# Optimization experiments

Measured on AMD Instinct MI355X. Metric: run time of the kernel, lower is better.

Reference implementation:

```python
import jax, jax.numpy as jnp
import numpy as np

N, H, M, B = 512, 64, 1024, 256
ETA = 1.0
INIT_STD = 0.01

def setup_inputs() -> dict:
    key = jax.random.key(0)
    k1, k2, k3, k4 = jax.random.split(key, 4)
    # Binary +/-1 sequences and memory (as produced upstream in the repo)
    sequences = jnp.where(jax.random.uniform(k1, (B, N)) < 0.5, -1.0, 1.0).astype(jnp.float32)
    memory = jnp.where(jax.random.uniform(k2, (M, N)) < 0.5, -1.0, 1.0).astype(jnp.float32)
    A_logits = (INIT_STD * jax.random.normal(k3, (N, H, N))).astype(jnp.float32)
    B_logits = (INIT_STD * jax.random.normal(k4, (H, N))).astype(jnp.float32)
    return {"sequences": sequences, "memory": memory, "A_logits": A_logits, "B_logits": B_logits}

def reference(sequences, memory, A_logits, B_logits):
    # Vectorized version of DAM.train_batch's loss over positions n=1..N-1.
    n_dim = sequences.shape[1]
    # Causal mask: row for position n attends to indices i < n. Rows n=1..N-1.
    ns = jnp.arange(1, n_dim)[:, None, None]            # (N-1,1,1)
    idx = jnp.arange(n_dim)[None, None, :]              # (1,1,N)
    mask = idx < ns                                      # (N-1,1,N)
    neg_inf = jnp.asarray(-jnp.inf, A_logits.dtype)
    A = jax.nn.softmax(jnp.where(mask, A_logits[1:], neg_inf), axis=-1)  # (N-1,H,N), zeros outside mask
    Bn = jax.nn.softmax(B_logits, axis=-1)               # (H,N)
    phi_mu = jnp.einsum('hn,mn->mh', Bn, memory)         # (M,H) memory keys
    hat_phi = jnp.einsum('bi,nhi->bnh', sequences, A)    # (B,N-1,H) queries for every position at once
    score = ETA * jnp.einsum('bnh,mh->bnm', hat_phi, phi_mu)  # (B,N-1,M)
    pi = jax.nn.softmax(score, axis=-1)                  # retrieval distribution over memories
    plus = (memory[:, 1:] > 0).astype(pi.dtype)          # (M,N-1): memory bit at position n is +1
    prob = jnp.einsum('bnm,mn->bn', pi, plus)            # P(next bit = +1)
    prob = jnp.clip(prob, 1e-6, 1.0 - 1e-6)
    target = (sequences[:, 1:] > 0).astype(prob.dtype)
    bce = -(target * jnp.log(prob) + (1.0 - target) * jnp.log1p(-prob))
    # mean over batch per position, summed over positions, / (N-1) == global mean
    return jnp.mean(bce)
```

## Files before the change

### kernel.cpp

```cpp
#include <hip/hip_runtime.h>
#include <stdint.h>

#define NPOS 512
#define NH   64
#define NM   1024
#define NB   256
#define NM1  511

typedef __attribute__((ext_vector_type(8)))  short bf16x8;
typedef __attribute__((ext_vector_type(16))) float f32x16;
typedef __attribute__((ext_vector_type(4)))  float f32x4;
typedef __attribute__((ext_vector_type(4)))  int   i32x4;

#if __has_builtin(__builtin_amdgcn_exp2f)
#define EXP2F(x) __builtin_amdgcn_exp2f(x)
#else
#define EXP2F(x) __expf((x) * 0.69314718055994531f)
#endif

__device__ __forceinline__ unsigned short f2bf(float x) {
    unsigned u = __float_as_uint(x);
    u = (u + 0x7FFFu + ((u >> 16) & 1u)) >> 16;
    return (unsigned short)u;
}
__device__ __forceinline__ int pack2(unsigned short a, unsigned short b) {
    return (int)a | ((int)b << 16);
}

__global__ __launch_bounds__(256, 4)
void kA_prep(const float* __restrict__ seq, const float* __restrict__ Bl,
             const float* __restrict__ mem,
             unsigned short* __restrict__ seq_bf, float* __restrict__ BnT,
             float* __restrict__ plusT, float* __restrict__ out) {
    const int bid = blockIdx.x, t = threadIdx.x;
    if (bid < 128) {
        if (bid == 0 && t == 0) out[0] = 0.f;
        int idx = (bid * 256 + t) * 4;
        f32x4 v = *(const f32x4*)(seq + idx);
        int2 o;
        o.x = pack2(f2bf(v.x), f2bf(v.y));
        o.y = pack2(f2bf(v.z), f2bf(v.w));
        *(int2*)(seq_bf + idx) = o;
    } else if (bid < 144) {
        const int h = (bid - 128) * 4 + (t >> 6), l = t & 63;
        float v[8]; float mx = -1e30f;
#pragma unroll
        for (int j = 0; j < 8; j++) { v[j] = Bl[h * NPOS + l + 64 * j]; mx = fmaxf(mx, v[j]); }
#pragma unroll
        for (int o = 32; o; o >>= 1) mx = fmaxf(mx, __shfl_xor(mx, o));
        float s = 0.f;
#pragma unroll
        for (int j = 0; j < 8; j++) { v[j] = __expf(v[j] - mx); s += v[j]; }
#pragma unroll
        for (int o = 32; o; o >>= 1) s += __shfl_xor(s, o);
        float r = 1.0f / s;
#pragma unroll
        for (int j = 0; j < 8; j++) BnT[(l + 64 * j) * NH + h] = v[j] * r;
    } else {
        __shared__ float sT[64][65];
        const int bb = bid - 144;
        const int mt = bb >> 3, nt = bb & 7;
        const int rr = t >> 2, cc = t & 3;
        const float* src = mem + (size_t)(mt * 64 + rr) * NPOS + nt * 64 + cc * 16;
#pragma unroll
        for (int j = 0; j < 4; j++) {
            f32x4 v = *(const f32x4*)(src + j * 4);
            sT[rr][cc * 16 + j * 4 + 0] = (v.x > 0.f) ? 1.f : 0.f;
            sT[rr][cc * 16 + j * 4 + 1] = (v.y > 0.f) ? 1.f : 0.f;
            sT[rr][cc * 16 + j * 4 + 2] = (v.z > 0.f) ? 1.f : 0.f;
            sT[rr][cc * 16 + j * 4 + 3] = (v.w > 0.f) ? 1.f : 0.f;
        }
        __syncthreads();
        float* dst = plusT + (size_t)(nt * 64 + rr) * NM + mt * 64 + cc * 16;
#pragma unroll
        for (int j = 0; j < 4; j++) {
            f32x4 o;
            o.x = sT[cc * 16 + j * 4 + 0][rr];
            o.y = sT[cc * 16 + j * 4 + 1][rr];
            o.z = sT[cc * 16 + j * 4 + 2][rr];
            o.w = sT[cc * 16 + j * 4 + 3][rr];
            *(f32x4*)(dst + j * 4) = o;
        }
    }
}

__global__ __launch_bounds__(256, 4)
void k1b_phimu(const float* __restrict__ BnT, const float* __restrict__ mem,
               unsigned short* __restrict__ phimu) {
    const int m0 = blockIdx.x * 2, t = threadIdx.x;
    __shared__ float mrow[2][NPOS];
    __shared__ float part[2][256];
    {
        int row = t >> 7, c = (t & 127) * 4;
        *(f32x4*)(&mrow[row][c]) = *(const f32x4*)(mem + (size_t)(m0 + row) * NPOS + c);
    }
    __syncthreads();
    const int h = t & 63, seg = t >> 6;
    float a[2] = {0.f, 0.f};
    float b2[2] = {0.f, 0.f};
    const float* bp = BnT + seg * 128 * NH + h;
#pragma unroll 8
    for (int nn = 0; nn < 128; nn += 2) {
        float x0 = bp[nn * NH], x1 = bp[(nn + 1) * NH];
#pragma unroll
        for (int row = 0; row < 2; row++) {
            a[row]  = fmaf(x0, mrow[row][seg * 128 + nn], a[row]);
            b2[row] = fmaf(x1, mrow[row][seg * 128 + nn + 1], b2[row]);
        }
    }
#pragma unroll
    for (int row = 0; row < 2; row++) part[row][t] = a[row] + b2[row];
    __syncthreads();
    if (t < 64) {
#pragma unroll
        for (int row = 0; row < 2; row++) {
            float s = (part[row][t] + part[row][t + 64]) + (part[row][t + 128] + part[row][t + 192]);
            phimu[(m0 + row) * NH + t] = f2bf(s * 1.4426950408889634f);
        }
    }
}

__global__ __launch_bounds__(256, 2)
void k23_fused(const float* __restrict__ Al, const unsigned short* __restrict__ seq_bf,
               const unsigned short* __restrict__ phimu, const float* __restrict__ plusT,
               const float* __restrict__ seq, float* __restrict__ out) {
    __shared__ __align__(16) unsigned short s_lds[256 * 72];
    __shared__ __align__(16) unsigned short e_lds[64 * 72];
    __shared__ float z_lds[64];
    __shared__ float s_plus[NM];

    const int t = threadIdx.x;
    const int n = NM1 - (int)blockIdx.x;
    const int ksteps = (n + 63) >> 6;
    const int wv = t >> 6, lane = t & 63, half = lane >> 5, r = lane & 31;

    if (t < 64) z_lds[t] = 0.f;
    *(f32x4*)(s_plus + t * 4) = *(const f32x4*)(plusT + n * NM + t * 4);

    const int eh = t >> 2, ei = (t & 3) * 16;
    const float* arow = Al + ((size_t)n * NH + eh) * NPOS + ei;
    const unsigned short* srcS = seq_bf + (size_t)t * NPOS;

    f32x16 acc00, acc01, acc10, acc11;
#pragma unroll
    for (int i = 0; i < 16; i++) { acc00[i] = 0.f; acc01[i] = 0.f; acc10[i] = 0.f; acc11[i] = 0.f; }

    f32x4 ea[4]; i32x4 sa[8];
#pragma unroll
    for (int g = 0; g < 4; g++) ea[g] = *(const f32x4*)(arow + g * 4);
#pragma unroll
    for (int c = 0; c < 8; c++) sa[c] = *(const i32x4*)(srcS + c * 8);
    __syncthreads();

    for (int kk = 0; kk < ksteps; kk++) {
        const int k0 = kk * 64;
        {
            float zp = 0.f;
            unsigned short* ep = e_lds + eh * 72 + ei;
#pragma unroll
            for (int g = 0; g < 4; g++) {
                int i0 = k0 + ei + g * 4;
                float e0 = (i0 + 0 < n) ? __expf(ea[g].x) : 0.f;
                float e1 = (i0 + 1 < n) ? __expf(ea[g].y) : 0.f;
                float e2 = (i0 + 2 < n) ? __expf(ea[g].z) : 0.f;
                float e3 = (i0 + 3 < n) ? __expf(ea[g].w) : 0.f;
                zp += (e0 + e1) + (e2 + e3);
                int2 o; o.x = pack2(f2bf(e0), f2bf(e1)); o.y = pack2(f2bf(e2), f2bf(e3));
                *(int2*)(ep + g * 4) = o;
            }
            zp += __shfl_xor(zp, 1);
            zp += __shfl_xor(zp, 2);
            if ((t & 3) == 0) z_lds[eh] += zp;
        }
        {
            unsigned short* dp = s_lds + t * 72;
#pragma unroll
            for (int c = 0; c < 8; c++) *(i32x4*)(dp + c * 8) = sa[c];
        }
        __syncthreads();
        if (kk + 1 < ksteps) {
#pragma unroll
            for (int g = 0; g < 4; g++) ea[g] = *(const f32x4*)(arow + k0 + 64 + g * 4);
#pragma unroll
            for (int c = 0; c < 8; c++) sa[c] = *(const i32x4*)(srcS + k0 + 64 + c * 8);
        }
        {
            const unsigned short* sA0 = s_lds + (wv * 64 + r) * 72;
            const unsigned short* sA1 = sA0 + 32 * 72;
            const unsigned short* sB0 = e_lds + r * 72;
            const unsigned short* sB1 = sB0 + 32 * 72;
#pragma unroll
            for (int kq = 0; kq < 4; kq++) {
                const int ko = kq * 16 + half * 8;
                bf16x8 A0 = *(const bf16x8*)(sA0 + ko);
                bf16x8 A1 = *(const bf16x8*)(sA1 + ko);
                bf16x8 B0 = *(const bf16x8*)(sB0 + ko);
                bf16x8 B1 = *(const bf16x8*)(sB1 + ko);
                acc00 = __builtin_amdgcn_mfma_f32_32x32x16_bf16(A0, B0, acc00, 0, 0, 0);
                acc01 = __builtin_amdgcn_mfma_f32_32x32x16_bf16(A0, B1, acc01, 0, 0, 0);
                acc10 = __builtin_amdgcn_mfma_f32_32x32x16_bf16(A1, B0, acc10, 0, 0, 0);
                acc11 = __builtin_amdgcn_mfma_f32_32x32x16_bf16(A1, B1, acc11, 0, 0, 0);
            }
        }
        __syncthreads();
    }
    {
        float rz0 = 1.0f / z_lds[r];
        float rz1 = 1.0f / z_lds[32 + r];
#pragma unroll
        for (int reg = 0; reg < 16; reg++) {
            int row = (reg & 3) + 8 * (reg >> 2) + 4 * half;
            s_lds[(wv * 64 + row) * 72 + r]            = f2bf(acc00[reg] * rz0);
            s_lds[(wv * 64 + row) * 72 + 32 + r]       = f2bf(acc01[reg] * rz1);
            s_lds[(wv * 64 + 32 + row) * 72 + r]       = f2bf(acc10[reg] * rz0);
            s_lds[(wv * 64 + 32 + row) * 72 + 32 + r]  = f2bf(acc11[reg] * rz1);
        }
    }
    __syncthreads();

    bf16x8 p[4];
#pragma unroll
    for (int kq = 0; kq < 4; kq++)
        p[kq] = *(const bf16x8*)(phimu + (r) * NH + kq * 16 + half * 8);
    bf16x8 q[2][4];
#pragma unroll
    for (int bs = 0; bs < 2; bs++)
#pragma unroll
        for (int kq = 0; kq < 4; kq++)
            q[bs][kq] = *(const bf16x8*)(s_lds + (wv * 64 + bs * 32 + r) * 72 + kq * 16 + half * 8);

    f32x4 den0 = {0.f,0.f,0.f,0.f}, num0 = {0.f,0.f,0.f,0.f};
    f32x4 den1 = {0.f,0.f,0.f,0.f}, num1 = {0.f,0.f,0.f,0.f};

    for (int it = 0; it < 32; ++it) {
        bf16x8 pn[4];
        if (it < 31) {
#pragma unroll
            for (int kq = 0; kq < 4; kq++)
                pn[kq] = *(const bf16x8*)(phimu + ((it + 1) * 32 + r) * NH + kq * 16 + half * 8);
        }
        f32x16 a0, a1;
#pragma unroll
        for (int i = 0; i < 16; i++) { a0[i] = 0.f; a1[i] = 0.f; }
#pragma unroll
        for (int kq = 0; kq < 4; kq++) {
            a0 = __builtin_amdgcn_mfma_f32_32x32x16_bf16(p[kq], q[0][kq], a0, 0, 0, 0);
            a1 = __builtin_amdgcn_mfma_f32_32x32x16_bf16(p[kq], q[1][kq], a1, 0, 0, 0);
        }
        const int mb = it * 32;
        f32x4 pv[4];
#pragma unroll
        for (int g = 0; g < 4; g++) pv[g] = *(const f32x4*)(s_plus + mb + 4 * half + 8 * g);
#pragma unroll
        for (int g = 0; g < 4; g++) {
            f32x4 e0, e1;
#pragma unroll
            for (int j = 0; j < 4; j++) {
                e0[j] = EXP2F(a0[4 * g + j]);
                e1[j] = EXP2F(a1[4 * g + j]);
            }
            den0 += e0; num0 += e0 * pv[g];
            den1 += e1; num1 += e1 * pv[g];
        }
        if (it < 31) {
#pragma unroll
            for (int kq = 0; kq < 4; kq++) p[kq] = pn[kq];
        }
    }
    float d0 = (den0[0] + den0[1]) + (den0[2] + den0[3]);
    float nu0 = (num0[0] + num0[1]) + (num0[2] + num0[3]);
    float d1 = (den1[0] + den1[1]) + (den1[2] + den1[3]);
    float nu1 = (num1[0] + num1[1]) + (num1[2] + num1[3]);
    d0 += __shfl_xor(d0, 32); nu0 += __shfl_xor(nu0, 32);
    d1 += __shfl_xor(d1, 32); nu1 += __shfl_xor(nu1, 32);

    float* dsum = (float*)e_lds;
    float* nsum = dsum + 256;
    if (half == 0) {
        dsum[wv * 64 + r]      = d0; nsum[wv * 64 + r]      = nu0;
        dsum[wv * 64 + 32 + r] = d1; nsum[wv * 64 + 32 + r] = nu1;
    }
    __syncthreads();
    {
        float dd = dsum[t], nn = nsum[t];
        float p2 = nn / dd;
        p2 = fminf(fmaxf(p2, 1e-6f), 1.0f - 1e-6f);
        float tg = seq[(size_t)t * NPOS + n];
        float bce = (tg > 0.f) ? -logf(p2) : -logf(1.0f - p2);
#pragma unroll
        for (int o = 32; o; o >>= 1) bce += __shfl_xor(bce, o);
        if (lane == 0) z_lds[wv] = bce;
    }
    __syncthreads();
    if (t == 0)
        atomicAdd(out, (z_lds[0] + z_lds[1] + z_lds[2] + z_lds[3]) * (1.0f / 130816.0f));
}

extern "C" void kernel_launch(void* const* d_in, const int* in_sizes, int n_in,
                              void* d_out, int out_size, void* d_ws, size_t ws_size,
                              hipStream_t stream) {
    const float* seq = (const float*)d_in[0];
    const float* mem = (const float*)d_in[1];
    const float* Al  = (const float*)d_in[2];
    const float* Bl  = (const float*)d_in[3];

    char* ws = (char*)d_ws;
    unsigned short* seq_bf = (unsigned short*)(ws + 0);
    float*          BnT    = (float*)(ws + 262144);
    unsigned short* phimu  = (unsigned short*)(ws + 393216);
    float*          plusT  = (float*)(ws + 524288);
    float*          outp   = (float*)d_out;

    kA_prep<<<272, 256, 0, stream>>>(seq, Bl, mem, seq_bf, BnT, plusT, outp);
    k1b_phimu<<<512, 256, 0, stream>>>(BnT, mem, phimu);
    k23_fused<<<511, 256, 0, stream>>>(Al, seq_bf, phimu, plusT, seq, outp);
}
```

Baseline: 145.6 us.

## Split batch across two blocks per position in fused attention-retrieval kernel

Each position is now processed by two blocks, each covering 128 batch rows, with one 32-row MFMA tile per wave instead of two. Launch bounds raise target occupancy to 4 blocks per CU and the grid doubles to 1022. The aim is better load balance of the triangular per-position workload and more latency hiding. In exchange, the softmax exponentials of A and the plus-vector loads are duplicated across the two blocks.

```diff
diff --git a/kernel.cpp b/kernel.cpp
--- a/kernel.cpp
+++ b/kernel.cpp
@@ -120,36 +120,39 @@
     }
 }
 
-__global__ __launch_bounds__(256, 2)
+__global__ __launch_bounds__(256, 4)
 void k23_fused(const float* __restrict__ Al, const unsigned short* __restrict__ seq_bf,
                const unsigned short* __restrict__ phimu, const float* __restrict__ plusT,
                const float* __restrict__ seq, float* __restrict__ out) {
-    __shared__ __align__(16) unsigned short s_lds[256 * 72];
+    __shared__ __align__(16) unsigned short s_lds[128 * 72];
     __shared__ __align__(16) unsigned short e_lds[64 * 72];
     __shared__ float z_lds[64];
     __shared__ float s_plus[NM];
 
     const int t = threadIdx.x;
-    const int n = NM1 - (int)blockIdx.x;
+    const int bid = blockIdx.x;
+    const int n = NM1 - (bid >> 1);
+    const int boff = (bid & 1) << 7;
     const int ksteps = (n + 63) >> 6;
     const int wv = t >> 6, lane = t & 63, half = lane >> 5, r = lane & 31;
 
     if (t < 64) z_lds[t] = 0.f;
-    *(f32x4*)(s_plus + t * 4) = *(const f32x4*)(plusT + n * NM + t * 4);
+    *(f32x4*)(s_plus + t * 4) = *(const f32x4*)(plusT + (size_t)n * NM + t * 4);
 
     const int eh = t >> 2, ei = (t & 3) * 16;
     const float* arow = Al + ((size_t)n * NH + eh) * NPOS + ei;
-    const unsigned short* srcS = seq_bf + (size_t)t * NPOS;
-
-    f32x16 acc00, acc01, acc10, acc11;
-#pragma unroll
-    for (int i = 0; i < 16; i++) { acc00[i] = 0.f; acc01[i] = 0.f; acc10[i] = 0.f; acc11[i] = 0.f; }
-
-    f32x4 ea[4]; i32x4 sa[8];
+    const int srow = t & 127, skh = (t >> 7) * 32;
+    const unsigned short* srcS = seq_bf + (size_t)(boff + srow) * NPOS + skh;
+
+    f32x16 acc0, acc1;
+#pragma unroll
+    for (int i = 0; i < 16; i++) { acc0[i] = 0.f; acc1[i] = 0.f; }
+
+    f32x4 ea[4]; i32x4 sa[4];
 #pragma unroll
     for (int g = 0; g < 4; g++) ea[g] = *(const f32x4*)(arow + g * 4);
 #pragma unroll
-    for (int c = 0; c < 8; c++) sa[c] = *(const i32x4*)(srcS + c * 8);
+    for (int c = 0; c < 4; c++) sa[c] = *(const i32x4*)(srcS + c * 8);
     __syncthreads();
 
     for (int kk = 0; kk < ksteps; kk++) {
@@ -173,33 +176,29 @@
             if ((t & 3) == 0) z_lds[eh] += zp;
         }
         {
-            unsigned short* dp = s_lds + t * 72;
-#pragma unroll
-            for (int c = 0; c < 8; c++) *(i32x4*)(dp + c * 8) = sa[c];
+            unsigned short* dp = s_lds + srow * 72 + skh;
+#pragma unroll
+            for (int c = 0; c < 4; c++) *(i32x4*)(dp + c * 8) = sa[c];
         }
         __syncthreads();
         if (kk + 1 < ksteps) {
 #pragma unroll
             for (int g = 0; g < 4; g++) ea[g] = *(const f32x4*)(arow + k0 + 64 + g * 4);
 #pragma unroll
-            for (int c = 0; c < 8; c++) sa[c] = *(const i32x4*)(srcS + k0 + 64 + c * 8);
+            for (int c = 0; c < 4; c++) sa[c] = *(const i32x4*)(srcS + k0 + 64 + c * 8);
         }
         {
-            const unsigned short* sA0 = s_lds + (wv * 64 + r) * 72;
-            const unsigned short* sA1 = sA0 + 32 * 72;
+            const unsigned short* sA  = s_lds + (wv * 32 + r) * 72;
             const unsigned short* sB0 = e_lds + r * 72;
             const unsigned short* sB1 = sB0 + 32 * 72;
 #pragma unroll
             for (int kq = 0; kq < 4; kq++) {
                 const int ko = kq * 16 + half * 8;
-                bf16x8 A0 = *(const bf16x8*)(sA0 + ko);
-                bf16x8 A1 = *(const bf16x8*)(sA1 + ko);
+                bf16x8 A0 = *(const bf16x8*)(sA + ko);
                 bf16x8 B0 = *(const bf16x8*)(sB0 + ko);
                 bf16x8 B1 = *(const bf16x8*)(sB1 + ko);
-                acc00 = __builtin_amdgcn_mfma_f32_32x32x16_bf16(A0, B0, acc00, 0, 0, 0);
-                acc01 = __builtin_amdgcn_mfma_f32_32x32x16_bf16(A0, B1, acc01, 0, 0, 0);
-                acc10 = __builtin_amdgcn_mfma_f32_32x32x16_bf16(A1, B0, acc10, 0, 0, 0);
-                acc11 = __builtin_amdgcn_mfma_f32_32x32x16_bf16(A1, B1, acc11, 0, 0, 0);
+                acc0 = __builtin_amdgcn_mfma_f32_32x32x16_bf16(A0, B0, acc0, 0, 0, 0);
+                acc1 = __builtin_amdgcn_mfma_f32_32x32x16_bf16(A0, B1, acc1, 0, 0, 0);
             }
         }
         __syncthreads();
@@ -210,27 +209,21 @@
 #pragma unroll
         for (int reg = 0; reg < 16; reg++) {
             int row = (reg & 3) + 8 * (reg >> 2) + 4 * half;
-            s_lds[(wv * 64 + row) * 72 + r]            = f2bf(acc00[reg] * rz0);
-            s_lds[(wv * 64 + row) * 72 + 32 + r]       = f2bf(acc01[reg] * rz1);
-            s_lds[(wv * 64 + 32 + row) * 72 + r]       = f2bf(acc10[reg] * rz0);
-            s_lds[(wv * 64 + 32 + row) * 72 + 32 + r]  = f2bf(acc11[reg] * rz1);
-        }
-    }
-    __syncthreads();
+            s_lds[(wv * 32 + row) * 72 + r]      = f2bf(acc0[reg] * rz0);
+            s_lds[(wv * 32 + row) * 72 + 32 + r] = f2bf(acc1[reg] * rz1);
+        }
+    }
 
     bf16x8 p[4];
 #pragma unroll
     for (int kq = 0; kq < 4; kq++)
-        p[kq] = *(const bf16x8*)(phimu + (r) * NH + kq * 16 + half * 8);
-    bf16x8 q[2][4];
-#pragma unroll
-    for (int bs = 0; bs < 2; bs++)
-#pragma unroll
-        for (int kq = 0; kq < 4; kq++)
-            q[bs][kq] = *(const bf16x8*)(s_lds + (wv * 64 + bs * 32 + r) * 72 + kq * 16 + half * 8);
-
-    f32x4 den0 = {0.f,0.f,0.f,0.f}, num0 = {0.f,0.f,0.f,0.f};
-    f32x4 den1 = {0.f,0.f,0.f,0.f}, num1 = {0.f,0.f,0.f,0.f};
+        p[kq] = *(const bf16x8*)(phimu + r * NH + kq * 16 + half * 8);
+    bf16x8 q[4];
+#pragma unroll
+    for (int kq = 0; kq < 4; kq++)
+        q[kq] = *(const bf16x8*)(s_lds + (wv * 32 + r) * 72 + kq * 16 + half * 8);
+
+    f32x4 den = {0.f,0.f,0.f,0.f}, num = {0.f,0.f,0.f,0.f};
 
     for (int it = 0; it < 32; ++it) {
         bf16x8 pn[4];
@@ -239,58 +232,45 @@
             for (int kq = 0; kq < 4; kq++)
                 pn[kq] = *(const bf16x8*)(phimu + ((it + 1) * 32 + r) * NH + kq * 16 + half * 8);
         }
-        f32x16 a0, a1;
-#pragma unroll
-        for (int i = 0; i < 16; i++) { a0[i] = 0.f; a1[i] = 0.f; }
-#pragma unroll
-        for (int kq = 0; kq < 4; kq++) {
-            a0 = __builtin_amdgcn_mfma_f32_32x32x16_bf16(p[kq], q[0][kq], a0, 0, 0, 0);
-            a1 = __builtin_amdgcn_mfma_f32_32x32x16_bf16(p[kq], q[1][kq], a1, 0, 0, 0);
-        }
+        f32x16 a0;
+#pragma unroll
+        for (int i = 0; i < 16; i++) a0[i] = 0.f;
+#pragma unroll
+        for (int kq = 0; kq < 4; kq++)
+            a0 = __builtin_amdgcn_mfma_f32_32x32x16_bf16(p[kq], q[kq], a0, 0, 0, 0);
         const int mb = it * 32;
-        f32x4 pv[4];
-#pragma unroll
-        for (int g = 0; g < 4; g++) pv[g] = *(const f32x4*)(s_plus + mb + 4 * half + 8 * g);
 #pragma unroll
         for (int g = 0; g < 4; g++) {
-            f32x4 e0, e1;
-#pragma unroll
-            for (int j = 0; j < 4; j++) {
-                e0[j] = EXP2F(a0[4 * g + j]);
-                e1[j] = EXP2F(a1[4 * g + j]);
-            }
-            den0 += e0; num0 += e0 * pv[g];
-            den1 += e1; num1 += e1 * pv[g];
+            f32x4 pv = *(const f32x4*)(s_plus + mb + 4 * half + 8 * g);
+            f32x4 e;
+#pragma unroll
+            for (int j = 0; j < 4; j++) e[j] = EXP2F(a0[4 * g + j]);
+            den += e; num += e * pv;
         }
         if (it < 31) {
 #pragma unroll
             for (int kq = 0; kq < 4; kq++) p[kq] = pn[kq];
         }
     }
-    float d0 = (den0[0] + den0[1]) + (den0[2] + den0[3]);
-    float nu0 = (num0[0] + num0[1]) + (num0[2] + num0[3]);
-    float d1 = (den1[0] + den1[1]) + (den1[2] + den1[3]);
-    float nu1 = (num1[0] + num1[1]) + (num1[2] + num1[3]);
-    d0 += __shfl_xor(d0, 32); nu0 += __shfl_xor(nu0, 32);
-    d1 += __shfl_xor(d1, 32); nu1 += __shfl_xor(nu1, 32);
+    float d  = (den[0] + den[1]) + (den[2] + den[3]);
+    float nu = (num[0] + num[1]) + (num[2] + num[3]);
+    d += __shfl_xor(d, 32); nu += __shfl_xor(nu, 32);
 
     float* dsum = (float*)e_lds;
-    float* nsum = dsum + 256;
-    if (half == 0) {
-        dsum[wv * 64 + r]      = d0; nsum[wv * 64 + r]      = nu0;
-        dsum[wv * 64 + 32 + r] = d1; nsum[wv * 64 + 32 + r] = nu1;
-    }
-    __syncthreads();
-    {
-        float dd = dsum[t], nn = nsum[t];
-        float p2 = nn / dd;
+    float* nsum = dsum + 128;
+    if (half == 0) { dsum[wv * 32 + r] = d; nsum[wv * 32 + r] = nu; }
+    __syncthreads();
+    float bce = 0.f;
+    if (t < 128) {
+        float dd = dsum[t], nn2 = nsum[t];
+        float p2 = nn2 / dd;
         p2 = fminf(fmaxf(p2, 1e-6f), 1.0f - 1e-6f);
-        float tg = seq[(size_t)t * NPOS + n];
-        float bce = (tg > 0.f) ? -logf(p2) : -logf(1.0f - p2);
-#pragma unroll
-        for (int o = 32; o; o >>= 1) bce += __shfl_xor(bce, o);
-        if (lane == 0) z_lds[wv] = bce;
-    }
+        float tg = seq[(size_t)(boff + t) * NPOS + n];
+        bce = (tg > 0.f) ? -logf(p2) : -logf(1.0f - p2);
+    }
+#pragma unroll
+    for (int o = 32; o; o >>= 1) bce += __shfl_xor(bce, o);
+    if (lane == 0) z_lds[wv] = bce;
     __syncthreads();
     if (t == 0)
         atomicAdd(out, (z_lds[0] + z_lds[1] + z_lds[2] + z_lds[3]) * (1.0f / 130816.0f));
@@ -313,5 +293,5 @@
 
     kA_prep<<<272, 256, 0, stream>>>(seq, Bl, mem, seq_bf, BnT, plusT, outp);
     k1b_phimu<<<512, 256, 0, stream>>>(BnT, mem, phimu);
-    k23_fused<<<511, 256, 0, stream>>>(Al, seq_bf, phimu, plusT, seq, outp);
-}
+    k23_fused<<<1022, 256, 0, stream>>>(Al, seq_bf, phimu, plusT, seq, outp);
+}
```

Result: slower. 179.5 us (+23.3%).

## Keep sequence operands in registers, double-buffer exp tiles, software-pipeline retrieval MFMAs

Applied to the files above, without the earlier changes.

Sequence tiles are now loaded from global memory straight into MFMA operand registers instead of being staged through LDS. The exponentiated A tile is double-buffered, so each k-step needs one barrier instead of two. The retrieval phase is software-pipelined so the MFMA for one phimu tile overlaps the exp/sum of the previous one. The aim is less LDS traffic and fewer barriers and stalls, at the cost of more registers. The final q writes to q_lds followed by reads from other rows have no barrier between them, since each wave reads only its own rows, which relies on the wave-local layout.

```diff
diff --git a/kernel.cpp b/kernel.cpp
--- a/kernel.cpp
+++ b/kernel.cpp
@@ -120,12 +120,45 @@
     }
 }
 
+__device__ __forceinline__ void p2_load(bf16x8 (&p)[4], const unsigned short* __restrict__ phimu,
+                                        int tile, int r, int half) {
+#pragma unroll
+    for (int kq = 0; kq < 4; kq++)
+        p[kq] = *(const bf16x8*)(phimu + (size_t)(tile * 32 + r) * NH + kq * 16 + half * 8);
+}
+__device__ __forceinline__ void p2_mfma(const bf16x8 (&p)[4], const bf16x8 (&q0)[4], const bf16x8 (&q1)[4],
+                                        f32x16& a0, f32x16& a1) {
+#pragma unroll
+    for (int i = 0; i < 16; i++) { a0[i] = 0.f; a1[i] = 0.f; }
+#pragma unroll
+    for (int kq = 0; kq < 4; kq++) {
+        a0 = __builtin_amdgcn_mfma_f32_32x32x16_bf16(p[kq], q0[kq], a0, 0, 0, 0);
+        a1 = __builtin_amdgcn_mfma_f32_32x32x16_bf16(p[kq], q1[kq], a1, 0, 0, 0);
+    }
+}
+__device__ __forceinline__ void p2_expsum(const f32x16& a0, const f32x16& a1, const float* s_plus,
+                                          int mb, int half,
+                                          f32x4& den0, f32x4& num0, f32x4& den1, f32x4& num1) {
+#pragma unroll
+    for (int g = 0; g < 4; g++) {
+        f32x4 pv = *(const f32x4*)(s_plus + mb + 4 * half + 8 * g);
+        f32x4 e0, e1;
+#pragma unroll
+        for (int j = 0; j < 4; j++) {
+            e0[j] = EXP2F(a0[4 * g + j]);
+            e1[j] = EXP2F(a1[4 * g + j]);
+        }
+        den0 += e0; num0 += e0 * pv;
+        den1 += e1; num1 += e1 * pv;
+    }
+}
+
 __global__ __launch_bounds__(256, 2)
 void k23_fused(const float* __restrict__ Al, const unsigned short* __restrict__ seq_bf,
                const unsigned short* __restrict__ phimu, const float* __restrict__ plusT,
                const float* __restrict__ seq, float* __restrict__ out) {
-    __shared__ __align__(16) unsigned short s_lds[256 * 72];
-    __shared__ __align__(16) unsigned short e_lds[64 * 72];
+    __shared__ __align__(16) unsigned short e_lds[2][64 * 72];
+    __shared__ __align__(16) unsigned short q_lds[256 * 72];
     __shared__ float z_lds[64];
     __shared__ float s_plus[NM];
 
@@ -135,28 +168,34 @@
     const int wv = t >> 6, lane = t & 63, half = lane >> 5, r = lane & 31;
 
     if (t < 64) z_lds[t] = 0.f;
-    *(f32x4*)(s_plus + t * 4) = *(const f32x4*)(plusT + n * NM + t * 4);
+    *(f32x4*)(s_plus + t * 4) = *(const f32x4*)(plusT + (size_t)n * NM + t * 4);
 
     const int eh = t >> 2, ei = (t & 3) * 16;
     const float* arow = Al + ((size_t)n * NH + eh) * NPOS + ei;
-    const unsigned short* srcS = seq_bf + (size_t)t * NPOS;
+    const unsigned short* s0 = seq_bf + (size_t)(wv * 64 + r) * NPOS;
+    const unsigned short* s1 = seq_bf + (size_t)(wv * 64 + 32 + r) * NPOS;
 
     f32x16 acc00, acc01, acc10, acc11;
 #pragma unroll
     for (int i = 0; i < 16; i++) { acc00[i] = 0.f; acc01[i] = 0.f; acc10[i] = 0.f; acc11[i] = 0.f; }
 
-    f32x4 ea[4]; i32x4 sa[8];
+    f32x4 ea[4];
+    bf16x8 sc0[4], sc1[4], sn0[4], sn1[4];
 #pragma unroll
     for (int g = 0; g < 4; g++) ea[g] = *(const f32x4*)(arow + g * 4);
 #pragma unroll
-    for (int c = 0; c < 8; c++) sa[c] = *(const i32x4*)(srcS + c * 8);
+    for (int kq = 0; kq < 4; kq++) {
+        sc0[kq] = *(const bf16x8*)(s0 + kq * 16 + half * 8);
+        sc1[kq] = *(const bf16x8*)(s1 + kq * 16 + half * 8);
+    }
     __syncthreads();
 
     for (int kk = 0; kk < ksteps; kk++) {
         const int k0 = kk * 64;
+        unsigned short* ebuf = e_lds[kk & 1];
         {
             float zp = 0.f;
-            unsigned short* ep = e_lds + eh * 72 + ei;
+            unsigned short* ep = ebuf + eh * 72 + ei;
 #pragma unroll
             for (int g = 0; g < 4; g++) {
                 int i0 = k0 + ei + g * 4;
@@ -172,37 +211,36 @@
             zp += __shfl_xor(zp, 2);
             if ((t & 3) == 0) z_lds[eh] += zp;
         }
+        if (kk + 1 < ksteps) {
+#pragma unroll
+            for (int g = 0; g < 4; g++) ea[g] = *(const f32x4*)(arow + k0 + 64 + g * 4);
+#pragma unroll
+            for (int kq = 0; kq < 4; kq++) {
+                sn0[kq] = *(const bf16x8*)(s0 + k0 + 64 + kq * 16 + half * 8);
+                sn1[kq] = *(const bf16x8*)(s1 + k0 + 64 + kq * 16 + half * 8);
+            }
+        }
+        asm volatile("s_waitcnt lgkmcnt(0)" ::: "memory");
+        __builtin_amdgcn_s_barrier();
+        asm volatile("" ::: "memory");
         {
-            unsigned short* dp = s_lds + t * 72;
-#pragma unroll
-            for (int c = 0; c < 8; c++) *(i32x4*)(dp + c * 8) = sa[c];
-        }
-        __syncthreads();
-        if (kk + 1 < ksteps) {
-#pragma unroll
-            for (int g = 0; g < 4; g++) ea[g] = *(const f32x4*)(arow + k0 + 64 + g * 4);
-#pragma unroll
-            for (int c = 0; c < 8; c++) sa[c] = *(const i32x4*)(srcS + k0 + 64 + c * 8);
-        }
-        {
-            const unsigned short* sA0 = s_lds + (wv * 64 + r) * 72;
-            const unsigned short* sA1 = sA0 + 32 * 72;
-            const unsigned short* sB0 = e_lds + r * 72;
+            const unsigned short* sB0 = ebuf + r * 72;
             const unsigned short* sB1 = sB0 + 32 * 72;
 #pragma unroll
             for (int kq = 0; kq < 4; kq++) {
                 const int ko = kq * 16 + half * 8;
-                bf16x8 A0 = *(const bf16x8*)(sA0 + ko);
-                bf16x8 A1 = *(const bf16x8*)(sA1 + ko);
                 bf16x8 B0 = *(const bf16x8*)(sB0 + ko);
                 bf16x8 B1 = *(const bf16x8*)(sB1 + ko);
-                acc00 = __builtin_amdgcn_mfma_f32_32x32x16_bf16(A0, B0, acc00, 0, 0, 0);
-                acc01 = __builtin_amdgcn_mfma_f32_32x32x16_bf16(A0, B1, acc01, 0, 0, 0);
-                acc10 = __builtin_amdgcn_mfma_f32_32x32x16_bf16(A1, B0, acc10, 0, 0, 0);
-                acc11 = __builtin_amdgcn_mfma_f32_32x32x16_bf16(A1, B1, acc11, 0, 0, 0);
+                acc00 = __builtin_amdgcn_mfma_f32_32x32x16_bf16(sc0[kq], B0, acc00, 0, 0, 0);
+                acc01 = __builtin_amdgcn_mfma_f32_32x32x16_bf16(sc0[kq], B1, acc01, 0, 0, 0);
+                acc10 = __builtin_amdgcn_mfma_f32_32x32x16_bf16(sc1[kq], B0, acc10, 0, 0, 0);
+                acc11 = __builtin_amdgcn_mfma_f32_32x32x16_bf16(sc1[kq], B1, acc11, 0, 0, 0);
             }
         }
-        __syncthreads();
+        if (kk + 1 < ksteps) {
+#pragma unroll
+            for (int kq = 0; kq < 4; kq++) { sc0[kq] = sn0[kq]; sc1[kq] = sn1[kq]; }
+        }
     }
     {
         float rz0 = 1.0f / z_lds[r];
@@ -210,63 +248,37 @@
 #pragma unroll
         for (int reg = 0; reg < 16; reg++) {
             int row = (reg & 3) + 8 * (reg >> 2) + 4 * half;
-            s_lds[(wv * 64 + row) * 72 + r]            = f2bf(acc00[reg] * rz0);
-            s_lds[(wv * 64 + row) * 72 + 32 + r]       = f2bf(acc01[reg] * rz1);
-            s_lds[(wv * 64 + 32 + row) * 72 + r]       = f2bf(acc10[reg] * rz0);
-            s_lds[(wv * 64 + 32 + row) * 72 + 32 + r]  = f2bf(acc11[reg] * rz1);
-        }
-    }
-    __syncthreads();
-
-    bf16x8 p[4];
-#pragma unroll
-    for (int kq = 0; kq < 4; kq++)
-        p[kq] = *(const bf16x8*)(phimu + (r) * NH + kq * 16 + half * 8);
-    bf16x8 q[2][4];
-#pragma unroll
-    for (int bs = 0; bs < 2; bs++)
-#pragma unroll
-        for (int kq = 0; kq < 4; kq++)
-            q[bs][kq] = *(const bf16x8*)(s_lds + (wv * 64 + bs * 32 + r) * 72 + kq * 16 + half * 8);
+            q_lds[(wv * 64 + row) * 72 + r]            = f2bf(acc00[reg] * rz0);
+            q_lds[(wv * 64 + row) * 72 + 32 + r]       = f2bf(acc01[reg] * rz1);
+            q_lds[(wv * 64 + 32 + row) * 72 + r]       = f2bf(acc10[reg] * rz0);
+            q_lds[(wv * 64 + 32 + row) * 72 + 32 + r]  = f2bf(acc11[reg] * rz1);
+        }
+    }
+
+    bf16x8 pA[4], pB[4];
+    p2_load(pA, phimu, 0, r, half);
+    p2_load(pB, phimu, 1, r, half);
+    bf16x8 q0[4], q1[4];
+#pragma unroll
+    for (int kq = 0; kq < 4; kq++) {
+        q0[kq] = *(const bf16x8*)(q_lds + (wv * 64 + r) * 72 + kq * 16 + half * 8);
+        q1[kq] = *(const bf16x8*)(q_lds + (wv * 64 + 32 + r) * 72 + kq * 16 + half * 8);
+    }
 
     f32x4 den0 = {0.f,0.f,0.f,0.f}, num0 = {0.f,0.f,0.f,0.f};
     f32x4 den1 = {0.f,0.f,0.f,0.f}, num1 = {0.f,0.f,0.f,0.f};
-
-    for (int it = 0; it < 32; ++it) {
-        bf16x8 pn[4];
-        if (it < 31) {
-#pragma unroll
-            for (int kq = 0; kq < 4; kq++)
-                pn[kq] = *(const bf16x8*)(phimu + ((it + 1) * 32 + r) * NH + kq * 16 + half * 8);
-        }
-        f32x16 a0, a1;
-#pragma unroll
-        for (int i = 0; i < 16; i++) { a0[i] = 0.f; a1[i] = 0.f; }
-#pragma unroll
-        for (int kq = 0; kq < 4; kq++) {
-            a0 = __builtin_amdgcn_mfma_f32_32x32x16_bf16(p[kq], q[0][kq], a0, 0, 0, 0);
-            a1 = __builtin_amdgcn_mfma_f32_32x32x16_bf16(p[kq], q[1][kq], a1, 0, 0, 0);
-        }
-        const int mb = it * 32;
-        f32x4 pv[4];
-#pragma unroll
-        for (int g = 0; g < 4; g++) pv[g] = *(const f32x4*)(s_plus + mb + 4 * half + 8 * g);
-#pragma unroll
-        for (int g = 0; g < 4; g++) {
-            f32x4 e0, e1;
-#pragma unroll
-            for (int j = 0; j < 4; j++) {
-                e0[j] = EXP2F(a0[4 * g + j]);
-                e1[j] = EXP2F(a1[4 * g + j]);
-            }
-            den0 += e0; num0 += e0 * pv[g];
-            den1 += e1; num1 += e1 * pv[g];
-        }
-        if (it < 31) {
-#pragma unroll
-            for (int kq = 0; kq < 4; kq++) p[kq] = pn[kq];
-        }
-    }
+    f32x16 aA0, aA1, aB0, aB1;
+
+    p2_mfma(pA, q0, q1, aA0, aA1);
+    for (int it = 0; it < 32; it += 2) {
+        if (it + 2 < 32) p2_load(pA, phimu, it + 2, r, half);
+        p2_mfma(pB, q0, q1, aB0, aB1);
+        if (it + 3 < 32) p2_load(pB, phimu, it + 3, r, half);
+        p2_expsum(aA0, aA1, s_plus, it * 32, half, den0, num0, den1, num1);
+        if (it + 2 < 32) p2_mfma(pA, q0, q1, aA0, aA1);
+        p2_expsum(aB0, aB1, s_plus, (it + 1) * 32, half, den0, num0, den1, num1);
+    }
+
     float d0 = (den0[0] + den0[1]) + (den0[2] + den0[3]);
     float nu0 = (num0[0] + num0[1]) + (num0[2] + num0[3]);
     float d1 = (den1[0] + den1[1]) + (den1[2] + den1[3]);
```

Result: no change. 148.4 us (+1.9%).

## Precompute masked exp of A_logits in prep kernel and pair blocks by workload

Applied to the files above, without the earlier changes.

Moves the masked exponentiation of A_logits into the prep kernel, writing bf16 exp values and per-head normalizers to workspace. The main kernel then streams these with register double-buffering and applies the 1/Z softmax scale after the first matmul instead of normalizing inline. Block order is interleaved so long and short causal positions alternate for load balance. The cost is an extra round trip of about 33MB of bf16 exp data through global memory. The new path only runs when the workspace is large enough.

```diff
diff --git a/kernel.cpp b/kernel.cpp
--- a/kernel.cpp
+++ b/kernel.cpp
@@ -26,6 +26,276 @@
 __device__ __forceinline__ int pack2(unsigned short a, unsigned short b) {
     return (int)a | ((int)b << 16);
 }
+
+
+__global__ __launch_bounds__(256, 4)
+void kAE_prep(const float* __restrict__ seq, const float* __restrict__ Bl,
+              const float* __restrict__ mem, const float* __restrict__ Al,
+              unsigned short* __restrict__ seq_bf, float* __restrict__ BnT,
+              float* __restrict__ plusT, unsigned short* __restrict__ Ew,
+              float* __restrict__ Zb, float* __restrict__ out) {
+    const int bid = blockIdx.x, t = threadIdx.x;
+    if (bid < 128) {
+        if (bid == 0 && t == 0) out[0] = 0.f;
+        int idx = (bid * 256 + t) * 4;
+        f32x4 v = *(const f32x4*)(seq + idx);
+        int2 o;
+        o.x = pack2(f2bf(v.x), f2bf(v.y));
+        o.y = pack2(f2bf(v.z), f2bf(v.w));
+        *(int2*)(seq_bf + idx) = o;
+    } else if (bid < 144) {
+        const int h = (bid - 128) * 4 + (t >> 6), l = t & 63;
+        float v[8]; float mx = -1e30f;
+#pragma unroll
+        for (int j = 0; j < 8; j++) { v[j] = Bl[h * NPOS + l + 64 * j]; mx = fmaxf(mx, v[j]); }
+#pragma unroll
+        for (int o = 32; o; o >>= 1) mx = fmaxf(mx, __shfl_xor(mx, o));
+        float s = 0.f;
+#pragma unroll
+        for (int j = 0; j < 8; j++) { v[j] = __expf(v[j] - mx); s += v[j]; }
+#pragma unroll
+        for (int o = 32; o; o >>= 1) s += __shfl_xor(s, o);
+        float r = 1.0f / s;
+#pragma unroll
+        for (int j = 0; j < 8; j++) BnT[(l + 64 * j) * NH + h] = v[j] * r;
+    } else if (bid < 272) {
+        __shared__ float sT[64][65];
+        const int bb = bid - 144;
+        const int mt = bb >> 3, nt = bb & 7;
+        const int rr = t >> 2, cc = t & 3;
+        const float* src = mem + (size_t)(mt * 64 + rr) * NPOS + nt * 64 + cc * 16;
+#pragma unroll
+        for (int j = 0; j < 4; j++) {
+            f32x4 v = *(const f32x4*)(src + j * 4);
+            sT[rr][cc * 16 + j * 4 + 0] = (v.x > 0.f) ? 1.f : 0.f;
+            sT[rr][cc * 16 + j * 4 + 1] = (v.y > 0.f) ? 1.f : 0.f;
+            sT[rr][cc * 16 + j * 4 + 2] = (v.z > 0.f) ? 1.f : 0.f;
+            sT[rr][cc * 16 + j * 4 + 3] = (v.w > 0.f) ? 1.f : 0.f;
+        }
+        __syncthreads();
+        float* dst = plusT + (size_t)(nt * 64 + rr) * NM + mt * 64 + cc * 16;
+#pragma unroll
+        for (int j = 0; j < 4; j++) {
+            f32x4 o;
+            o.x = sT[cc * 16 + j * 4 + 0][rr];
+            o.y = sT[cc * 16 + j * 4 + 1][rr];
+            o.z = sT[cc * 16 + j * 4 + 2][rr];
+            o.w = sT[cc * 16 + j * 4 + 3][rr];
+            *(f32x4*)(dst + j * 4) = o;
+        }
+    } else {
+        const int n = bid - 271;
+        const int h = t >> 2, j = t & 3;
+        const int lim = ((n + 63) >> 6) * 64;
+        const float* Ar = Al + ((size_t)n * NH + h) * NPOS;
+        unsigned short* Er = Ew + (size_t)(n - 1) * 32768 + h * 64;
+        float zp = 0.f;
+#pragma unroll 4
+        for (int g = 0; g < 16; g++) {
+            const int i0 = g * 32 + j * 8;
+            if (g * 32 >= lim) break;
+            f32x4 v0 = *(const f32x4*)(Ar + i0);
+            f32x4 v1 = *(const f32x4*)(Ar + i0 + 4);
+            float e0 = (i0 + 0 < n) ? __expf(v0.x) : 0.f;
+            float e1 = (i0 + 1 < n) ? __expf(v0.y) : 0.f;
+            float e2 = (i0 + 2 < n) ? __expf(v0.z) : 0.f;
+            float e3 = (i0 + 3 < n) ? __expf(v0.w) : 0.f;
+            float e4 = (i0 + 4 < n) ? __expf(v1.x) : 0.f;
+            float e5 = (i0 + 5 < n) ? __expf(v1.y) : 0.f;
+            float e6 = (i0 + 6 < n) ? __expf(v1.z) : 0.f;
+            float e7 = (i0 + 7 < n) ? __expf(v1.w) : 0.f;
+            zp += ((e0 + e1) + (e2 + e3)) + ((e4 + e5) + (e6 + e7));
+            i32x4 w;
+            w.x = pack2(f2bf(e0), f2bf(e1));
+            w.y = pack2(f2bf(e2), f2bf(e3));
+            w.z = pack2(f2bf(e4), f2bf(e5));
+            w.w = pack2(f2bf(e6), f2bf(e7));
+            *(i32x4*)(Er + (i0 >> 6) * 4096 + (i0 & 63)) = w;
+        }
+        zp += __shfl_xor(zp, 1);
+        zp += __shfl_xor(zp, 2);
+        if (j == 0) Zb[(n - 1) * 64 + h] = zp;
+    }
+}
+
+__device__ __forceinline__ void p2_load(bf16x8 (&p)[4], const unsigned short* __restrict__ phimu,
+                                        int tile, int r, int half) {
+#pragma unroll
+    for (int kq = 0; kq < 4; kq++)
+        p[kq] = *(const bf16x8*)(phimu + (size_t)(tile * 32 + r) * NH + kq * 16 + half * 8);
+}
+__device__ __forceinline__ void p2_mfma(const bf16x8 (&p)[4], const bf16x8 (&q0)[4], const bf16x8 (&q1)[4],
+                                        const f32x16& z, f32x16& a0, f32x16& a1) {
+    a0 = __builtin_amdgcn_mfma_f32_32x32x16_bf16(p[0], q0[0], z, 0, 0, 0);
+    a1 = __builtin_amdgcn_mfma_f32_32x32x16_bf16(p[0], q1[0], z, 0, 0, 0);
+#pragma unroll
+    for (int kq = 1; kq < 4; kq++) {
+        a0 = __builtin_amdgcn_mfma_f32_32x32x16_bf16(p[kq], q0[kq], a0, 0, 0, 0);
+        a1 = __builtin_amdgcn_mfma_f32_32x32x16_bf16(p[kq], q1[kq], a1, 0, 0, 0);
+    }
+}
+__device__ __forceinline__ void p2_expsum(const f32x16& a0, const f32x16& a1, const float* s_plus,
+                                          int mb, int half,
+                                          f32x4& den0, f32x4& num0, f32x4& den1, f32x4& num1) {
+#pragma unroll
+    for (int g = 0; g < 4; g++) {
+        f32x4 pv = *(const f32x4*)(s_plus + mb + 4 * half + 8 * g);
+        f32x4 e0, e1;
+#pragma unroll
+        for (int j = 0; j < 4; j++) {
+            e0[j] = EXP2F(a0[4 * g + j]);
+            e1[j] = EXP2F(a1[4 * g + j]);
+        }
+        den0 += e0; num0 += e0 * pv;
+        den1 += e1; num1 += e1 * pv;
+    }
+}
+
+__global__ __launch_bounds__(256, 2)
+void k23_fusedE(const unsigned short* __restrict__ Ew, const float* __restrict__ Zb,
+                const unsigned short* __restrict__ seq_bf,
+                const unsigned short* __restrict__ phimu, const float* __restrict__ plusT,
+                const float* __restrict__ seq, float* __restrict__ out) {
+    __shared__ __align__(16) unsigned short e_lds[2][64 * 72];
+    __shared__ __align__(16) unsigned short q_lds[256 * 72];
+    __shared__ float s_plus[NM];
+    __shared__ float w_lds[4];
+
+    const int t = threadIdx.x;
+    const int c = blockIdx.x >> 1;
+    const int n = (blockIdx.x & 1) ? (1 + c) : (NM1 - c);
+    const int ksteps = (n + 63) >> 6;
+    const int wv = t >> 6, lane = t & 63, half = lane >> 5, r = lane & 31;
+
+    *(f32x4*)(s_plus + t * 4) = *(const f32x4*)(plusT + (size_t)n * NM + t * 4);
+    const float Zr0 = Zb[(n - 1) * 64 + r];
+    const float Zr1 = Zb[(n - 1) * 64 + 32 + r];
+
+    const unsigned short* Eb = Ew + (size_t)(n - 1) * 32768;
+    const int eh = t >> 2, ec = (t & 3) * 16;
+    const unsigned short* s0 = seq_bf + (size_t)(wv * 64 + r) * NPOS;
+    const unsigned short* s1 = seq_bf + (size_t)(wv * 64 + 32 + r) * NPOS;
+
+    f32x16 acc00, acc01, acc10, acc11;
+#pragma unroll
+    for (int i = 0; i < 16; i++) { acc00[i] = 0.f; acc01[i] = 0.f; acc10[i] = 0.f; acc11[i] = 0.f; }
+
+    bf16x8 er0, er1, sc0[4], sc1[4], sn0[4], sn1[4];
+    er0 = *(const bf16x8*)(Eb + eh * 64 + ec);
+    er1 = *(const bf16x8*)(Eb + eh * 64 + ec + 8);
+#pragma unroll
+    for (int kq = 0; kq < 4; kq++) {
+        sc0[kq] = *(const bf16x8*)(s0 + kq * 16 + half * 8);
+        sc1[kq] = *(const bf16x8*)(s1 + kq * 16 + half * 8);
+    }
+
+    for (int kk = 0; kk < ksteps; kk++) {
+        {
+            unsigned short* ep = (unsigned short*)e_lds[kk & 1] + eh * 72 + ec;
+            *(bf16x8*)(ep)     = er0;
+            *(bf16x8*)(ep + 8) = er1;
+        }
+        if (kk + 1 < ksteps) {
+            const unsigned short* nb = Eb + (kk + 1) * 4096 + eh * 64 + ec;
+            er0 = *(const bf16x8*)(nb);
+            er1 = *(const bf16x8*)(nb + 8);
+            const int k0 = (kk + 1) * 64;
+#pragma unroll
+            for (int kq = 0; kq < 4; kq++) {
+                sn0[kq] = *(const bf16x8*)(s0 + k0 + kq * 16 + half * 8);
+                sn1[kq] = *(const bf16x8*)(s1 + k0 + kq * 16 + half * 8);
+            }
+        }
+        asm volatile("s_waitcnt lgkmcnt(0)" ::: "memory");
+        __builtin_amdgcn_s_barrier();
+        asm volatile("" ::: "memory");
+        {
+            const unsigned short* sB0 = (const unsigned short*)e_lds[kk & 1] + r * 72;
+            const unsigned short* sB1 = sB0 + 32 * 72;
+#pragma unroll
+            for (int kq = 0; kq < 4; kq++) {
+                const int ko = kq * 16 + half * 8;
+                bf16x8 B0 = *(const bf16x8*)(sB0 + ko);
+                bf16x8 B1 = *(const bf16x8*)(sB1 + ko);
+                acc00 = __builtin_amdgcn_mfma_f32_32x32x16_bf16(sc0[kq], B0, acc00, 0, 0, 0);
+                acc01 = __builtin_amdgcn_mfma_f32_32x32x16_bf16(sc0[kq], B1, acc01, 0, 0, 0);
+                acc10 = __builtin_amdgcn_mfma_f32_32x32x16_bf16(sc1[kq], B0, acc10, 0, 0, 0);
+                acc11 = __builtin_amdgcn_mfma_f32_32x32x16_bf16(sc1[kq], B1, acc11, 0, 0, 0);
+            }
+        }
+        if (kk + 1 < ksteps) {
+#pragma unroll
+            for (int kq = 0; kq < 4; kq++) { sc0[kq] = sn0[kq]; sc1[kq] = sn1[kq]; }
+        }
+    }
+    {
+        float rz0 = 1.0f / Zr0;
+        float rz1 = 1.0f / Zr1;
+#pragma unroll
+        for (int reg = 0; reg < 16; reg++) {
+            int row = (reg & 3) + 8 * (reg >> 2) + 4 * half;
+            q_lds[(wv * 64 + row) * 72 + r]            = f2bf(acc00[reg] * rz0);
+            q_lds[(wv * 64 + row) * 72 + 32 + r]       = f2bf(acc01[reg] * rz1);
+            q_lds[(wv * 64 + 32 + row) * 72 + r]       = f2bf(acc10[reg] * rz0);
+            q_lds[(wv * 64 + 32 + row) * 72 + 32 + r]  = f2bf(acc11[reg] * rz1);
+        }
+    }
+
+    bf16x8 p[4], pn[4];
+    p2_load(p, phimu, 0, r, half);
+    bf16x8 q0[4], q1[4];
+#pragma unroll
+    for (int kq = 0; kq < 4; kq++) {
+        q0[kq] = *(const bf16x8*)(q_lds + (wv * 64 + r) * 72 + kq * 16 + half * 8);
+        q1[kq] = *(const bf16x8*)(q_lds + (wv * 64 + 32 + r) * 72 + kq * 16 + half * 8);
+    }
+    f32x16 zacc;
+#pragma unroll
+    for (int i = 0; i < 16; i++) zacc[i] = 0.f;
+
+    f32x4 den0 = {0.f,0.f,0.f,0.f}, num0 = {0.f,0.f,0.f,0.f};
+    f32x4 den1 = {0.f,0.f,0.f,0.f}, num1 = {0.f,0.f,0.f,0.f};
+    f32x16 a0, a1;
+
+    for (int it = 0; it < 32; ++it) {
+        if (it < 31) p2_load(pn, phimu, it + 1, r, half);
+        p2_mfma(p, q0, q1, zacc, a0, a1);
+        p2_expsum(a0, a1, s_plus, it * 32, half, den0, num0, den1, num1);
+        if (it < 31) {
+#pragma unroll
+            for (int kq = 0; kq < 4; kq++) p[kq] = pn[kq];
+        }
+    }
+
+    float d0 = (den0[0] + den0[1]) + (den0[2] + den0[3]);
+    float nu0 = (num0[0] + num0[1]) + (num0[2] + num0[3]);
+    float d1 = (den1[0] + den1[1]) + (den1[2] + den1[3]);
+    float nu1 = (num1[0] + num1[1]) + (num1[2] + num1[3]);
+    d0 += __shfl_xor(d0, 32); nu0 += __shfl_xor(nu0, 32);
+    d1 += __shfl_xor(d1, 32); nu1 += __shfl_xor(nu1, 32);
+
+    float* dsum = (float*)e_lds;
+    float* nsum = dsum + 256;
+    if (half == 0) {
+        dsum[wv * 64 + r]      = d0; nsum[wv * 64 + r]      = nu0;
+        dsum[wv * 64 + 32 + r] = d1; nsum[wv * 64 + 32 + r] = nu1;
+    }
+    __syncthreads();
+    {
+        float dd = dsum[t], nn = nsum[t];
+        float p2 = nn / dd;
+        p2 = fminf(fmaxf(p2, 1e-6f), 1.0f - 1e-6f);
+        float tg = seq[(size_t)t * NPOS + n];
+        float bce = (tg > 0.f) ? -logf(p2) : -logf(1.0f - p2);
+#pragma unroll
+        for (int o = 32; o; o >>= 1) bce += __shfl_xor(bce, o);
+        if (lane == 0) w_lds[wv] = bce;
+    }
+    __syncthreads();
+    if (t == 0)
+        atomicAdd(out, (w_lds[0] + w_lds[1] + w_lds[2] + w_lds[3]) * (1.0f / 130816.0f));
+}
+
 
 __global__ __launch_bounds__(256, 4)
 void kA_prep(const float* __restrict__ seq, const float* __restrict__ Bl,
@@ -84,46 +354,10 @@
     }
 }
 
-__global__ __launch_bounds__(256, 4)
-void k1b_phimu(const float* __restrict__ BnT, const float* __restrict__ mem,
-               unsigned short* __restrict__ phimu) {
-    const int m0 = blockIdx.x * 2, t = threadIdx.x;
-    __shared__ float mrow[2][NPOS];
-    __shared__ float part[2][256];
-    {
-        int row = t >> 7, c = (t & 127) * 4;
-        *(f32x4*)(&mrow[row][c]) = *(const f32x4*)(mem + (size_t)(m0 + row) * NPOS + c);
-    }
-    __syncthreads();
-    const int h = t & 63, seg = t >> 6;
-    float a[2] = {0.f, 0.f};
-    float b2[2] = {0.f, 0.f};
-    const float* bp = BnT + seg * 128 * NH + h;
-#pragma unroll 8
-    for (int nn = 0; nn < 128; nn += 2) {
-        float x0 = bp[nn * NH], x1 = bp[(nn + 1) * NH];
-#pragma unroll
-        for (int row = 0; row < 2; row++) {
-            a[row]  = fmaf(x0, mrow[row][seg * 128 + nn], a[row]);
-            b2[row] = fmaf(x1, mrow[row][seg * 128 + nn + 1], b2[row]);
-        }
-    }
-#pragma unroll
-    for (int row = 0; row < 2; row++) part[row][t] = a[row] + b2[row];
-    __syncthreads();
-    if (t < 64) {
-#pragma unroll
-        for (int row = 0; row < 2; row++) {
-            float s = (part[row][t] + part[row][t + 64]) + (part[row][t + 128] + part[row][t + 192]);
-            phimu[(m0 + row) * NH + t] = f2bf(s * 1.4426950408889634f);
-        }
-    }
-}
-
 __global__ __launch_bounds__(256, 2)
-void k23_fused(const float* __restrict__ Al, const unsigned short* __restrict__ seq_bf,
-               const unsigned short* __restrict__ phimu, const float* __restrict__ plusT,
-               const float* __restrict__ seq, float* __restrict__ out) {
+void k23_fused0(const float* __restrict__ Al, const unsigned short* __restrict__ seq_bf,
+                const unsigned short* __restrict__ phimu, const float* __restrict__ plusT,
+                const float* __restrict__ seq, float* __restrict__ out) {
     __shared__ __align__(16) unsigned short s_lds[256 * 72];
     __shared__ __align__(16) unsigned short e_lds[64 * 72];
     __shared__ float z_lds[64];
@@ -296,6 +530,42 @@
         atomicAdd(out, (z_lds[0] + z_lds[1] + z_lds[2] + z_lds[3]) * (1.0f / 130816.0f));
 }
 
+__global__ __launch_bounds__(256, 4)
+void k1b_phimu(const float* __restrict__ BnT, const float* __restrict__ mem,
+               unsigned short* __restrict__ phimu) {
+    const int m0 = blockIdx.x * 2, t = threadIdx.x;
+    __shared__ float mrow[2][NPOS];
+    __shared__ float part[2][256];
+    {
+        int row = t >> 7, c = (t & 127) * 4;
+        *(f32x4*)(&mrow[row][c]) = *(const f32x4*)(mem + (size_t)(m0 + row) * NPOS + c);
+    }
+    __syncthreads();
+    const int h = t & 63, seg = t >> 6;
+    float a[2] = {0.f, 0.f};
+    float b2[2] = {0.f, 0.f};
+    const float* bp = BnT + seg * 128 * NH + h;
+#pragma unroll 8
+    for (int nn = 0; nn < 128; nn += 2) {
+        float x0 = bp[nn * NH], x1 = bp[(nn + 1) * NH];
+#pragma unroll
+        for (int row = 0; row < 2; row++) {
+            a[row]  = fmaf(x0, mrow[row][seg * 128 + nn], a[row]);
+            b2[row] = fmaf(x1, mrow[row][seg * 128 + nn + 1], b2[row]);
+        }
+    }
+#pragma unroll
+    for (int row = 0; row < 2; row++) part[row][t] = a[row] + b2[row];
+    __syncthreads();
+    if (t < 64) {
+#pragma unroll
+        for (int row = 0; row < 2; row++) {
+            float s = (part[row][t] + part[row][t + 64]) + (part[row][t + 128] + part[row][t + 192]);
+            phimu[(m0 + row) * NH + t] = f2bf(s * 1.4426950408889634f);
+        }
+    }
+}
+
 extern "C" void kernel_launch(void* const* d_in, const int* in_sizes, int n_in,
                               void* d_out, int out_size, void* d_ws, size_t ws_size,
                               hipStream_t stream) {
@@ -309,9 +579,19 @@
     float*          BnT    = (float*)(ws + 262144);
     unsigned short* phimu  = (unsigned short*)(ws + 393216);
     float*          plusT  = (float*)(ws + 524288);
+    float*          Zb     = (float*)(ws + 2621440);
+    unsigned short* Ew     = (unsigned short*)(ws + 2752512);
     float*          outp   = (float*)d_out;
 
-    kA_prep<<<272, 256, 0, stream>>>(seq, Bl, mem, seq_bf, BnT, plusT, outp);
-    k1b_phimu<<<512, 256, 0, stream>>>(BnT, mem, phimu);
-    k23_fused<<<511, 256, 0, stream>>>(Al, seq_bf, phimu, plusT, seq, outp);
-}
+    const size_t WS_NEEDED_E = 2752512 + (size_t)NM1 * 32768 * sizeof(unsigned short);
+
+    if (ws_size >= WS_NEEDED_E) {
+        kAE_prep<<<783, 256, 0, stream>>>(seq, Bl, mem, Al, seq_bf, BnT, plusT, Ew, Zb, outp);
+        k1b_phimu<<<512, 256, 0, stream>>>(BnT, mem, phimu);
+        k23_fusedE<<<511, 256, 0, stream>>>(Ew, Zb, seq_bf, phimu, plusT, seq, outp);
+    } else {
+        kA_prep<<<272, 256, 0, stream>>>(seq, Bl, mem, seq_bf, BnT, plusT, outp);
+        k1b_phimu<<<512, 256, 0, stream>>>(BnT, mem, phimu);
+        k23_fused0<<<511, 256, 0, stream>>>(Al, seq_bf, phimu, plusT, seq, outp);
+    }
+}
```

Measured after the change: 158.9 us. 1.09x slower.
